# Optimization experiments

Measured on AMD Instinct MI355X. Metric: run time of the kernel, lower is better.

Reference implementation:

```python
import jax, jax.numpy as jnp
import numpy as np

NA, NT = 50000, 100000          # address / transaction node counts
FA, FT = 128, 64                # raw feature dims per node type
HID, OUT, HEADS, NCLS = 128, 64, 8, 2
E1, E2 = 500000, 250000         # cross-type / same-type edge counts
NEG_SLOPE = 0.2
LN_EPS = 1e-5


def _edge_att(xs, xd, src, dst, a_s, a_d, n_dst):
    # xs: [Ns,H,D] projected src feats, xd: [Nd,H,D] projected dst feats
    alpha_s = (xs * a_s).sum(-1)                     # [Ns,H]
    alpha_d = (xd * a_d).sum(-1)                     # [Nd,H]
    alpha = alpha_s[src] + alpha_d[dst]              # [E,H]
    alpha = jnp.where(alpha > 0, alpha, NEG_SLOPE * alpha)  # leaky_relu(0.2)
    # segment softmax over incoming edges of each dst node
    m = jax.lax.stop_gradient(jax.ops.segment_max(alpha, dst, num_segments=n_dst))
    m = jnp.where(jnp.isfinite(m), m, 0.0)
    ex = jnp.exp(alpha - m[dst])
    denom = jax.ops.segment_sum(ex, dst, num_segments=n_dst)
    w = ex / jnp.maximum(denom[dst], 1e-16)          # [E,H]
    msg = xs[src] * w[:, :, None]                    # [E,H,D]
    out = jax.ops.segment_sum(msg, dst, num_segments=n_dst)
    return jax.nn.relu(out.reshape(n_dst, -1))       # [Nd, H*D] (HANConv relu per edge type)


def _group(outs, q, kW, kb):
    # semantic-level attention over metapaths; outs: [K,N,F]
    score = (jnp.tanh(outs @ kW + kb).mean(axis=1) * q).sum(-1)  # [K]
    attn = jax.nn.softmax(score)
    return jnp.einsum('k,knf->nf', attn, outs)


def _layer_norm(x, g, b):
    mu = x.mean(-1, keepdims=True)
    var = ((x - mu) ** 2).mean(-1, keepdims=True)
    return (x - mu) / jnp.sqrt(var + LN_EPS) * g + b


def _han_conv(xa, xt, edges, Wa, ba, Wt, bt, atts, q, kW, kb):
    C = Wa.shape[1]
    D = C // HEADS
    za = (xa @ Wa + ba).reshape(-1, HEADS, D)
    zt = (xt @ Wt + bt).reshape(-1, HEADS, D)
    (eat_s, eat_d), (eta_s, eta_d), (eaa_s, eaa_d), (ett_s, ett_d) = edges
    (as_at, ad_at), (as_ta, ad_ta), (as_aa, ad_aa), (as_tt, ad_tt) = atts
    o_at = _edge_att(za, zt, eat_s, eat_d, as_at, ad_at, zt.shape[0])  # -> transaction
    o_ta = _edge_att(zt, za, eta_s, eta_d, as_ta, ad_ta, za.shape[0])  # -> address
    o_aa = _edge_att(za, za, eaa_s, eaa_d, as_aa, ad_aa, za.shape[0])  # -> address
    o_tt = _edge_att(zt, zt, ett_s, ett_d, as_tt, ad_tt, zt.shape[0])  # -> transaction
    new_a = _group(jnp.stack([o_ta, o_aa]), q, kW, kb)
    new_t = _group(jnp.stack([o_at, o_tt]), q, kW, kb)
    return new_a, new_t


def _forward(x_address, x_transaction,
             W_a1, b_a1, W_t1, b_t1,
             as_at1, ad_at1, as_ta1, ad_ta1, as_aa1, ad_aa1, as_tt1, ad_tt1,
             k1_W, k1_b, q1,
             W_a2, b_a2, W_t2, b_t2,
             as_at2, ad_at2, as_ta2, ad_ta2, as_aa2, ad_aa2, as_tt2, ad_tt2,
             k2_W, k2_b, q2,
             ln1_g, ln1_b, ln2_g, ln2_b, lin_W, lin_b, edges):
    atts1 = ((as_at1, ad_at1), (as_ta1, ad_ta1), (as_aa1, ad_aa1), (as_tt1, ad_tt1))
    atts2 = ((as_at2, ad_at2), (as_ta2, ad_ta2), (as_aa2, ad_aa2), (as_tt2, ad_tt2))
    xa, xt = _han_conv(x_address, x_transaction, edges, W_a1, b_a1, W_t1, b_t1, atts1, q1, k1_W, k1_b)
    xa = jax.nn.relu(_layer_norm(xa, ln1_g, ln1_b))
    xt = jax.nn.relu(_layer_norm(xt, ln1_g, ln1_b))
    # dropout is identity in eval mode
    xa, xt = _han_conv(xa, xt, edges, W_a2, b_a2, W_t2, b_t2, atts2, q2, k2_W, k2_b)
    xa = jax.nn.relu(_layer_norm(xa, ln2_g, ln2_b))
    return xa @ lin_W + lin_b                          # [NA, NCLS]


def setup_inputs() -> dict:
    key = jax.random.key(0)
    ks = jax.random.split(key, 40)
    D1, D2 = HID // HEADS, OUT // HEADS
    def n(i, shape, s=0.1):
        return jax.random.normal(ks[i], shape, jnp.float32) * s
    inp = {
        'x_address': jax.random.normal(ks[0], (NA, FA), jnp.float32),
        'x_transaction': jax.random.normal(ks[1], (NT, FT), jnp.float32),
        'eat_src': jax.random.randint(ks[2], (E1,), 0, NA),
        'eat_dst': jax.random.randint(ks[3], (E1,), 0, NT),
        'eta_src': jax.random.randint(ks[4], (E1,), 0, NT),
        'eta_dst': jax.random.randint(ks[5], (E1,), 0, NA),
        'eaa_src': jax.random.randint(ks[6], (E2,), 0, NA),
        'eaa_dst': jax.random.randint(ks[7], (E2,), 0, NA),
        'ett_src': jax.random.randint(ks[8], (E2,), 0, NT),
        'ett_dst': jax.random.randint(ks[9], (E2,), 0, NT),
        'W_a1': n(10, (FA, HID)), 'b_a1': jnp.zeros((HID,), jnp.float32),
        'W_t1': n(11, (FT, HID)), 'b_t1': jnp.zeros((HID,), jnp.float32),
        'as_at1': n(12, (HEADS, D1)), 'ad_at1': n(13, (HEADS, D1)),
        'as_ta1': n(14, (HEADS, D1)), 'ad_ta1': n(15, (HEADS, D1)),
        'as_aa1': n(16, (HEADS, D1)), 'ad_aa1': n(17, (HEADS, D1)),
        'as_tt1': n(18, (HEADS, D1)), 'ad_tt1': n(19, (HEADS, D1)),
        'k1_W': n(20, (HID, HID)), 'k1_b': jnp.zeros((HID,), jnp.float32), 'q1': n(21, (HID,)),
        'W_a2': n(22, (HID, OUT)), 'b_a2': jnp.zeros((OUT,), jnp.float32),
        'W_t2': n(23, (HID, OUT)), 'b_t2': jnp.zeros((OUT,), jnp.float32),
        'as_at2': n(24, (HEADS, D2)), 'ad_at2': n(25, (HEADS, D2)),
        'as_ta2': n(26, (HEADS, D2)), 'ad_ta2': n(27, (HEADS, D2)),
        'as_aa2': n(28, (HEADS, D2)), 'ad_aa2': n(29, (HEADS, D2)),
        'as_tt2': n(30, (HEADS, D2)), 'ad_tt2': n(31, (HEADS, D2)),
        'k2_W': n(32, (OUT, OUT)), 'k2_b': jnp.zeros((OUT,), jnp.float32), 'q2': n(33, (OUT,)),
        'ln1_g': jnp.ones((HID,), jnp.float32), 'ln1_b': jnp.zeros((HID,), jnp.float32),
        'ln2_g': jnp.ones((OUT,), jnp.float32), 'ln2_b': jnp.zeros((OUT,), jnp.float32),
        'lin_W': n(34, (OUT, NCLS)), 'lin_b': jnp.zeros((NCLS,), jnp.float32),
    }
    return inp


def reference(x_address, x_transaction,
              eat_src, eat_dst, eta_src, eta_dst, eaa_src, eaa_dst, ett_src, ett_dst,
              W_a1, b_a1, W_t1, b_t1,
              as_at1, ad_at1, as_ta1, ad_ta1, as_aa1, ad_aa1, as_tt1, ad_tt1,
              k1_W, k1_b, q1,
              W_a2, b_a2, W_t2, b_t2,
              as_at2, ad_at2, as_ta2, ad_ta2, as_aa2, ad_aa2, as_tt2, ad_tt2,
              k2_W, k2_b, q2,
              ln1_g, ln1_b, ln2_g, ln2_b, lin_W, lin_b):
    edges = ((eat_src, eat_dst), (eta_src, eta_dst), (eaa_src, eaa_dst), (ett_src, ett_dst))
    return _forward(x_address, x_transaction,
                    W_a1, b_a1, W_t1, b_t1,
                    as_at1, ad_at1, as_ta1, ad_ta1, as_aa1, ad_aa1, as_tt1, ad_tt1,
                    k1_W, k1_b, q1,
                    W_a2, b_a2, W_t2, b_t2,
                    as_at2, ad_at2, as_ta2, ad_ta2, as_aa2, ad_aa2, as_tt2, ad_tt2,
                    k2_W, k2_b, q2,
                    ln1_g, ln1_b, ln2_g, ln2_b, lin_W, lin_b, edges)
```

## Files before the change

### kernel.cpp

```cpp
#include <hip/hip_runtime.h>
#include <cstdint>
#include <cstddef>
#include <type_traits>

#define NA 50000
#define NT 100000
#define FA 128
#define FT 64
#define HID 128
#define OUTF 64
#define HEADS 8
#define E1 500000
#define E2 250000
#define NTOT (2*NT + 2*NA)
#define ETOT (2*E1 + 2*E2)
#define NSH 8

typedef __attribute__((ext_vector_type(8))) short short8;
typedef __attribute__((ext_vector_type(4))) float f32x4;

static __device__ __forceinline__ ushort f2b(float f) {
  unsigned int u = __float_as_uint(f);
  return (ushort)((u + 0x7fffu + ((u >> 16) & 1u)) >> 16);
}
static __device__ __forceinline__ float b2f(ushort b) {
  return __uint_as_float(((unsigned int)b) << 16);
}
static __device__ __forceinline__ float u2f_lo(unsigned int u) {
  return __uint_as_float(u << 16);
}
static __device__ __forceinline__ float u2f_hi(unsigned int u) {
  return __uint_as_float(u & 0xffff0000u);
}

template<int KK>
static __device__ __forceinline__ int lidx(int row, int off) {
  return row * KK + (off ^ ((row & 7) << 3));
}

template<int KK, int M>
static __device__ __forceinline__ void stageB(const float* __restrict__ W,
                                              ushort* __restrict__ Bls)
{
  constexpr int TPC = 256 / M;
  constexpr int CH  = KK / TPC;
  constexpr int BL  = (CH < 16) ? CH : 16;
  int t = threadIdx.x;
  int col = t % M;
  int k0 = (t / M) * CH;
  const float* Wp = W + col;
#pragma unroll
  for (int b = 0; b < CH; b += BL) {
    float v[BL];
#pragma unroll
    for (int i = 0; i < BL; i++) v[i] = Wp[(size_t)(k0 + b + i) * M];
#pragma unroll
    for (int q = 0; q < BL / 8; q++) {
      union { ushort u[8]; uint4 x; } p;
#pragma unroll
      for (int i = 0; i < 8; i++) p.u[i] = f2b(v[q * 8 + i]);
      *reinterpret_cast<uint4*>(&Bls[lidx<KK>(col, k0 + b + q * 8)]) = p.x;
    }
  }
}

template<int KK, typename AT>
struct ARegs {
  float4 f[std::is_same<AT, float>::value ? KK / 16 : 1];
  uint4  u[std::is_same<AT, float>::value ? 1 : KK / 32];
};

template<int KK, typename AT>
static __device__ __forceinline__ void loadA(const AT* __restrict__ A, int N,
                                             int row0, ARegs<KK, AT>& R)
{
  int t = threadIdx.x;
  int arow = t >> 2, ac0 = (t & 3) * (KK / 4);
  int row = row0 + arow;
  bool ok = row < N;
  const AT* Ap = A + (size_t)row * KK + ac0;
  if constexpr (std::is_same<AT, float>::value) {
#pragma unroll
    for (int j = 0; j < KK / 16; j++)
      R.f[j] = ok ? *reinterpret_cast<const float4*>(Ap + j * 4)
                  : make_float4(0.f, 0.f, 0.f, 0.f);
  } else {
#pragma unroll
    for (int j = 0; j < KK / 32; j++)
      R.u[j] = ok ? *reinterpret_cast<const uint4*>(Ap + j * 8)
                  : make_uint4(0, 0, 0, 0);
  }
}

template<int KK, typename AT>
static __device__ __forceinline__ void writeA(const ARegs<KK, AT>& R,
                                              ushort* __restrict__ Als)
{
  int t = threadIdx.x;
  int arow = t >> 2, ac0 = (t & 3) * (KK / 4);
#pragma unroll
  for (int j = 0; j < KK / 32; j++) {
    uint4 w;
    if constexpr (std::is_same<AT, float>::value) {
      union { ushort u[8]; uint4 x; } p;
      float4 a0 = R.f[2 * j], a1 = R.f[2 * j + 1];
      p.u[0] = f2b(a0.x); p.u[1] = f2b(a0.y); p.u[2] = f2b(a0.z); p.u[3] = f2b(a0.w);
      p.u[4] = f2b(a1.x); p.u[5] = f2b(a1.y); p.u[6] = f2b(a1.z); p.u[7] = f2b(a1.w);
      w = p.x;
    } else {
      w = R.u[j];
    }
    *reinterpret_cast<uint4*>(&Als[lidx<KK>(arow, ac0 + j * 8)]) = w;
  }
}

template<int KK, int NCT>
static __device__ __forceinline__ void mfma_tile(const ushort* __restrict__ Als,
    const ushort* __restrict__ Bls, f32x4* acc)
{
  int lane = threadIdx.x & 63, w = threadIdx.x >> 6;
  int l15 = lane & 15, l4 = lane >> 4;
#pragma unroll
  for (int ks = 0; ks < KK / 32; ks++) {
    short8 af = *reinterpret_cast<const short8*>(
        &Als[lidx<KK>(16 * w + l15, ks * 32 + l4 * 8)]);
#pragma unroll
    for (int n = 0; n < NCT; n++) {
      short8 bf = *reinterpret_cast<const short8*>(
          &Bls[lidx<KK>(16 * n + l15, ks * 32 + l4 * 8)]);
      acc[n] = __builtin_amdgcn_mfma_f32_16x16x32_bf16(af, bf, acc[n], 0, 0, 0);
    }
  }
}

template<int NV, int DD, int KK, int M, int TPB, typename AT>
__global__ __launch_bounds__(256) void zgemm_k(
    const AT* __restrict__ A, const float* __restrict__ W,
    const float* __restrict__ bias,
    const float* __restrict__ v0, const float* __restrict__ v1,
    const float* __restrict__ v2, const float* __restrict__ v3,
    float* __restrict__ o0, float* __restrict__ o1,
    float* __restrict__ o2, float* __restrict__ o3,
    ushort* __restrict__ Cb, int N)
{
  constexpr int NCT = M / 16;
  __shared__ __align__(16) ushort Bls[M * KK];
  __shared__ __align__(16) ushort Als[64 * KK];
  int t = threadIdx.x, w = t >> 6, lane = t & 63;
  int l15 = lane & 15, l4 = lane >> 4;
  int ntiles = (N + 63) >> 6;
  int tile0 = blockIdx.x * TPB;
  int nt = min(TPB, ntiles - tile0);

  stageB<KK, M>(W, Bls);
  ARegs<KK, AT> R;
  loadA<KK, AT>(A, N, tile0 * 64, R);

  float bv[NCT], aw0[NCT], aw1[NCT], aw2[NCT], aw3[NCT];
#pragma unroll
  for (int n = 0; n < NCT; n++) {
    int col = 16 * n + l15;
    bv[n] = bias[col];
    int head = (DD == 16) ? n : (n * 2 + (l15 >> 3));
    int vi = head * DD + (l15 & (DD - 1));
    aw0[n] = v0[vi];
    aw1[n] = (NV > 1) ? v1[vi] : 0.f;
    aw2[n] = (NV > 2) ? v2[vi] : 0.f;
    aw3[n] = (NV > 3) ? v3[vi] : 0.f;
  }

  for (int i = 0; i < nt; i++) {
    int row0 = (tile0 + i) * 64;
    __syncthreads();
    writeA<KK, AT>(R, Als);
    __syncthreads();
    if (i + 1 < nt) loadA<KK, AT>(A, N, row0 + 64, R);
    f32x4 acc[NCT];
#pragma unroll
    for (int n = 0; n < NCT; n++) acc[n] = (f32x4){0.f, 0.f, 0.f, 0.f};
    mfma_tile<KK, NCT>(Als, Bls, acc);

#pragma unroll
    for (int n = 0; n < NCT; n++) {
      int col = 16 * n + l15;
      int head = (DD == 16) ? n : (n * 2 + (l15 >> 3));
#pragma unroll
      for (int r = 0; r < 4; r++) {
        int row = row0 + 16 * w + l4 * 4 + r;
        float v = acc[n][r] + bv[n];
        if (row < N) Cb[(size_t)row * M + col] = f2b(v);
        float a0 = v * aw0[n], a1 = v * aw1[n], a2 = v * aw2[n], a3 = v * aw3[n];
#pragma unroll
        for (int o = 1; o < DD; o <<= 1) {
          a0 += __shfl_xor(a0, o);
          if (NV > 1) a1 += __shfl_xor(a1, o);
          if (NV > 2) a2 += __shfl_xor(a2, o);
          if (NV > 3) a3 += __shfl_xor(a3, o);
        }
        if ((l15 & (DD - 1)) == 0 && row < N) {
          o0[(size_t)row * 8 + head] = a0;
          if (NV > 1) o1[(size_t)row * 8 + head] = a1;
          if (NV > 2) o2[(size_t)row * 8 + head] = a2;
          if (NV > 3) o3[(size_t)row * 8 + head] = a3;
        }
      }
    }
  }
}

template<int KK, int M, int TPB>
__global__ __launch_bounds__(256) void score_k(
    const ushort* __restrict__ A0, const ushort* __restrict__ A1,
    const ushort* __restrict__ A2, const ushort* __restrict__ A3,
    const float* __restrict__ W, const float* __restrict__ bias,
    const float* __restrict__ qv, float* __restrict__ scp,
    int4 cumB, int4 Ns)
{
  constexpr int NCT = M / 16;
  __shared__ __align__(16) ushort Bls[M * KK];
  __shared__ __align__(16) ushort Als[64 * KK];
  __shared__ float red[4];
  int b = blockIdx.x;
  int tsk, bbase, N; const ushort* A;
  if      (b < cumB.x) { tsk = 0; bbase = 0;      N = Ns.x; A = A0; }
  else if (b < cumB.y) { tsk = 1; bbase = cumB.x; N = Ns.y; A = A1; }
  else if (b < cumB.z) { tsk = 2; bbase = cumB.y; N = Ns.z; A = A2; }
  else                 { tsk = 3; bbase = cumB.z; N = Ns.w; A = A3; }
  int t = threadIdx.x, w = t >> 6, lane = t & 63;
  int l15 = lane & 15, l4 = lane >> 4;
  int ntiles = (N + 63) >> 6;
  int tile0 = (b - bbase) * TPB;
  int nt = min(TPB, ntiles - tile0);

  stageB<KK, M>(W, Bls);
  ARegs<KK, ushort> R;
  loadA<KK, ushort>(A, N, tile0 * 64, R);

  float bb[NCT], qb[NCT];
#pragma unroll
  for (int n = 0; n < NCT; n++) {
    int col = 16 * n + l15;
    bb[n] = bias[col]; qb[n] = qv[col];
  }

  float ls = 0.f;
  for (int i = 0; i < nt; i++) {
    int row0 = (tile0 + i) * 64;
    __syncthreads();
    writeA<KK, ushort>(R, Als);
    __syncthreads();
    if (i + 1 < nt) loadA<KK, ushort>(A, N, row0 + 64, R);
    f32x4 acc[NCT];
#pragma unroll
    for (int n = 0; n < NCT; n++) acc[n] = (f32x4){0.f, 0.f, 0.f, 0.f};
    mfma_tile<KK, NCT>(Als, Bls, acc);
#pragma unroll
    for (int n = 0; n < NCT; n++) {
#pragma unroll
      for (int r = 0; r < 4; r++) {
        int row = row0 + 16 * w + l4 * 4 + r;
        if (row < N) ls += tanhf(acc[n][r] + bb[n]) * qb[n];
      }
    }
  }
#pragma unroll
  for (int o = 32; o > 0; o >>= 1) ls += __shfl_xor(ls, o);
  if (lane == 0) red[w] = ls;
  __syncthreads();
  if (t == 0) atomicAdd(&scp[tsk], red[0] + red[1] + red[2] + red[3]);
}

__global__ void hist4_sh(const int* __restrict__ d0, const int* __restrict__ d1,
    const int* __restrict__ d2, const int* __restrict__ d3,
    int* __restrict__ cnt8, float* __restrict__ scp)
{
  if (blockIdx.x == 0 && threadIdx.x < 8) scp[threadIdx.x] = 0.f;
  int e = blockIdx.x * 256 + threadIdx.x;
  int sh = blockIdx.x & (NSH - 1);
  int d;
  if      (e < E1)          d = d0[e];
  else if (e < 2*E1)        d = d1[e - E1] + NT;
  else if (e < 2*E1 + E2)   d = d2[e - 2*E1] + NT + NA;
  else if (e < ETOT)        d = d3[e - 2*E1 - E2] + NT + 2*NA;
  else return;
  atomicAdd(&cnt8[sh * NTOT + d], 1);
}

__global__ void scatter_sh(const int* __restrict__ s0, const int* __restrict__ d0,
    const int* __restrict__ s1, const int* __restrict__ d1,
    const int* __restrict__ s2, const int* __restrict__ d2,
    const int* __restrict__ s3, const int* __restrict__ d3,
    int* __restrict__ cur8, int* __restrict__ ssh)
{
  int e = blockIdx.x * 256 + threadIdx.x;
  int sh = blockIdx.x & (NSH - 1);
  int d, s;
  if      (e < E1)          { d = d0[e];                           s = s0[e]; }
  else if (e < 2*E1)        { d = d1[e - E1] + NT;                 s = s1[e - E1]; }
  else if (e < 2*E1 + E2)   { d = d2[e - 2*E1] + NT + NA;          s = s2[e - 2*E1]; }
  else if (e < ETOT)        { d = d3[e - 2*E1 - E2] + NT + 2*NA;   s = s3[e - 2*E1 - E2]; }
  else return;
  int p = atomicAdd(&cur8[sh * NTOT + d], 1);
  ssh[p] = s;
}

__global__ void compact_k(const int* __restrict__ rp8, const int* __restrict__ rp,
    const int* __restrict__ ssh, int* __restrict__ ssrc)
{
  int g = blockIdx.x * 256 + threadIdx.x;
  if (g >= NTOT) return;
  int w = rp[g];
#pragma unroll
  for (int s = 0; s < NSH; s++) {
    int b0 = rp8[s * NTOT + g], b1 = rp8[s * NTOT + g + 1];
    for (int e = b0; e < b1; e++) ssrc[w++] = ssh[e];
  }
}

__global__ __launch_bounds__(256) void scan_blk(const int* __restrict__ in,
    int* __restrict__ rp1, int* __restrict__ bsum, int n)
{
  __shared__ int sh[256];
  int base = blockIdx.x * 2048;
  int t = threadIdx.x;
  int v[8]; int s = 0;
#pragma unroll
  for (int k = 0; k < 8; k++) {
    int i = base + t * 8 + k;
    v[k] = (i < n) ? in[i] : 0; s += v[k];
  }
  sh[t] = s; __syncthreads();
  for (int o = 1; o < 256; o <<= 1) {
    int x = (t >= o) ? sh[t - o] : 0;
    __syncthreads(); sh[t] += x; __syncthreads();
  }
  int run = (t == 0) ? 0 : sh[t - 1];
  if (t == 255 && bsum) bsum[blockIdx.x] = sh[255];
#pragma unroll
  for (int k = 0; k < 8; k++) {
    int i = base + t * 8 + k;
    run += v[k];
    if (i < n) rp1[i] = run;
  }
}

__global__ __launch_bounds__(256) void scan_blk_sum8(const int* __restrict__ cnt8,
    int* __restrict__ rp1, int* __restrict__ bsum, int n)
{
  __shared__ int sh[256];
  int base = blockIdx.x * 2048;
  int t = threadIdx.x;
  int v[8]; int s = 0;
#pragma unroll
  for (int k = 0; k < 8; k++) {
    int i = base + t * 8 + k;
    int x = 0;
    if (i < n) {
#pragma unroll
      for (int sh2 = 0; sh2 < NSH; sh2++) x += cnt8[sh2 * NTOT + i];
    }
    v[k] = x; s += x;
  }
  sh[t] = s; __syncthreads();
  for (int o = 1; o < 256; o <<= 1) {
    int x = (t >= o) ? sh[t - o] : 0;
    __syncthreads(); sh[t] += x; __syncthreads();
  }
  int run = (t == 0) ? 0 : sh[t - 1];
  if (t == 255 && bsum) bsum[blockIdx.x] = sh[255];
#pragma unroll
  for (int k = 0; k < 8; k++) {
    int i = base + t * 8 + k;
    run += v[k];
    if (i < n) rp1[i] = run;
  }
}

__global__ __launch_bounds__(256) void scan_two(int* __restrict__ b0, int n0,
                                                int* __restrict__ b1, int n1)
{
  __shared__ int sh[256];
  int* arr = blockIdx.x ? b1 : b0;
  int n = blockIdx.x ? n1 : n0;
  int t = threadIdx.x;
  int v[8]; int s = 0;
#pragma unroll
  for (int k = 0; k < 8; k++) {
    int i = t * 8 + k;
    v[k] = (i < n) ? arr[i] : 0; s += v[k];
  }
  sh[t] = s; __syncthreads();
  for (int o = 1; o < 256; o <<= 1) {
    int x = (t >= o) ? sh[t - o] : 0;
    __syncthreads(); sh[t] += x; __syncthreads();
  }
  int run = (t == 0) ? 0 : sh[t - 1];
#pragma unroll
  for (int k = 0; k < 8; k++) {
    int i = t * 8 + k;
    run += v[k];
    if (i < n) arr[i] = run;
  }
}

__global__ void scan_add2(int* __restrict__ rp, int* __restrict__ cur,
    const int* __restrict__ bsA, int n)
{
  int i = blockIdx.x * blockDim.x + threadIdx.x;
  if (i == 0) { rp[0] = 0; cur[0] = 0; }
  if (i < n) {
    int blk = i >> 11;
    int base = blk ? bsA[blk - 1] : 0;
    int v = rp[i + 1] + base;
    rp[i + 1] = v;
    if (i + 1 < n) cur[i + 1] = v;
  }
}

__global__ void scan_add(int* __restrict__ rp, const int* __restrict__ bsA, int n)
{
  int i = blockIdx.x * blockDim.x + threadIdx.x;
  if (i == 0) rp[0] = 0;
  if (i < n) {
    int blk = i >> 11;
    int base = blk ? bsA[blk - 1] : 0;
    rp[i + 1] += base;
  }
}

struct AggTask {
  int g0, Nd;
  const float* als; const float* ald;
  const ushort* z;  ushort* out;
};

template<int F>
__global__ __launch_bounds__(256) void agg_multi(const int* __restrict__ rp,
    const int* __restrict__ ssrc, AggTask C0A, AggTask C0B,
    AggTask C1A, AggTask C1B, int split0, int split1, int btot)
{
  constexpr int LPN = (F == 128) ? 16 : 8;
  constexpr int NPW = 64 / LPN;
  int b = blockIdx.x;
  int cls = (b >> 2) & 1;
  int lb = (b >> 3) * 4 + (b & 3);
  if (lb >= btot) return;
  AggTask T;
  if (cls == 0) { if (lb < split0) T = C0A; else { T = C0B; lb -= split0; } }
  else          { if (lb < split1) T = C1A; else { T = C1B; lb -= split1; } }
  int wv = threadIdx.x >> 6, lane = threadIdx.x & 63;
  int grp = lane / LPN, lg = lane % LPN;
  int n = (lb * 4 + wv) * NPW + grp;
  if (n >= T.Nd) return;
  int g = T.g0 + n;
  int start = rp[g], end = rp[g + 1];
  int hh = (F == 128) ? (lg >> 1) : lg;
  float ad_h = T.ald[(size_t)n * 8 + hh];

  float den = 0.f;
  float acc[8] = {};
  int e = start;
  for (; e + 1 < end; e += 2) {
    int sn0 = ssrc[e], sn1 = ssrc[e + 1];
    uint4 z0 = *reinterpret_cast<const uint4*>(T.z + (size_t)sn0 * F + lg * 8);
    uint4 z1 = *reinterpret_cast<const uint4*>(T.z + (size_t)sn1 * F + lg * 8);
    float a0 = T.als[(size_t)sn0 * 8 + hh] + ad_h;
    float a1 = T.als[(size_t)sn1 * 8 + hh] + ad_h;
    a0 = a0 > 0.f ? a0 : 0.2f * a0;
    a1 = a1 > 0.f ? a1 : 0.2f * a1;
    float p0 = __expf(fminf(a0, 30.f));
    float p1 = __expf(fminf(a1, 30.f));
    den += p0 + p1;
    acc[0] = fmaf(p0, u2f_lo(z0.x), fmaf(p1, u2f_lo(z1.x), acc[0]));
    acc[1] = fmaf(p0, u2f_hi(z0.x), fmaf(p1, u2f_hi(z1.x), acc[1]));
    acc[2] = fmaf(p0, u2f_lo(z0.y), fmaf(p1, u2f_lo(z1.y), acc[2]));
    acc[3] = fmaf(p0, u2f_hi(z0.y), fmaf(p1, u2f_hi(z1.y), acc[3]));
    acc[4] = fmaf(p0, u2f_lo(z0.z), fmaf(p1, u2f_lo(z1.z), acc[4]));
    acc[5] = fmaf(p0, u2f_hi(z0.z), fmaf(p1, u2f_hi(z1.z), acc[5]));
    acc[6] = fmaf(p0, u2f_lo(z0.w), fmaf(p1, u2f_lo(z1.w), acc[6]));
    acc[7] = fmaf(p0, u2f_hi(z0.w), fmaf(p1, u2f_hi(z1.w), acc[7]));
  }
  if (e < end) {
    int sn = ssrc[e];
    uint4 zv = *reinterpret_cast<const uint4*>(T.z + (size_t)sn * F + lg * 8);
    float a = T.als[(size_t)sn * 8 + hh] + ad_h;
    a = a > 0.f ? a : 0.2f * a;
    float p = __expf(fminf(a, 30.f));
    den += p;
    acc[0] = fmaf(p, u2f_lo(zv.x), acc[0]);
    acc[1] = fmaf(p, u2f_hi(zv.x), acc[1]);
    acc[2] = fmaf(p, u2f_lo(zv.y), acc[2]);
    acc[3] = fmaf(p, u2f_hi(zv.y), acc[3]);
    acc[4] = fmaf(p, u2f_lo(zv.z), acc[4]);
    acc[5] = fmaf(p, u2f_hi(zv.z), acc[5]);
    acc[6] = fmaf(p, u2f_lo(zv.w), acc[6]);
    acc[7] = fmaf(p, u2f_hi(zv.w), acc[7]);
  }
  float inv = 1.f / fmaxf(den, 1e-16f);
  unsigned int pk[4];
#pragma unroll
  for (int k2 = 0; k2 < 4; k2++)
    pk[k2] = (unsigned int)f2b(fmaxf(acc[2*k2] * inv, 0.f))
           | ((unsigned int)f2b(fmaxf(acc[2*k2+1] * inv, 0.f)) << 16);
  *reinterpret_cast<uint4*>(T.out + (size_t)n * F + lg * 8)
      = make_uint4(pk[0], pk[1], pk[2], pk[3]);
}

__global__ __launch_bounds__(256) void combine2_k(
    const ushort* __restrict__ o00, const ushort* __restrict__ o01,
    const float* __restrict__ sc0, float invn0, ushort* __restrict__ out0, int N0,
    const ushort* __restrict__ o10, const ushort* __restrict__ o11,
    const float* __restrict__ sc1, float invn1, ushort* __restrict__ out1, int N1,
    const float* __restrict__ g, const float* __restrict__ bb)
{
  int c1 = (N0 + 3) / 4;
  int b = blockIdx.x;
  const ushort *o0, *o1; const float* sc; float invn; ushort* outp; int N, lb;
  if (b < c1) { o0=o00; o1=o01; sc=sc0; invn=invn0; outp=out0; N=N0; lb=b; }
  else        { o0=o10; o1=o11; sc=sc1; invn=invn1; outp=out1; N=N1; lb=b-c1; }
  int wv = threadIdx.x >> 6, lane = threadIdx.x & 63;
  int n = lb * 4 + wv;
  if (n >= N) return;
  float s0 = sc[0] * invn, s1 = sc[1] * invn;
  float mx = fmaxf(s0, s1);
  float e0 = __expf(s0 - mx), e1 = __expf(s1 - mx);
  float w0 = e0 / (e0 + e1), w1 = e1 / (e0 + e1);
  float x[2];
#pragma unroll
  for (int jj = 0; jj < 2; jj++) {
    int idx = lane + 64 * jj;
    x[jj] = w0 * b2f(o0[(size_t)n * 128 + idx]) + w1 * b2f(o1[(size_t)n * 128 + idx]);
  }
  float sum = x[0] + x[1];
#pragma unroll
  for (int o = 32; o > 0; o >>= 1) sum += __shfl_xor(sum, o);
  float mu = sum / 128.f;
  float vs = 0.f;
#pragma unroll
  for (int jj = 0; jj < 2; jj++) { float dd = x[jj] - mu; vs = fmaf(dd, dd, vs); }
#pragma unroll
  for (int o = 32; o > 0; o >>= 1) vs += __shfl_xor(vs, o);
  float rstd = rsqrtf(vs / 128.f + 1e-5f);
#pragma unroll
  for (int jj = 0; jj < 2; jj++) {
    int idx = lane + 64 * jj;
    float y = (x[jj] - mu) * rstd * g[idx] + bb[idx];
    outp[(size_t)n * 128 + idx] = f2b(fmaxf(y, 0.f));
  }
}

__global__ __launch_bounds__(256) void combine_final_k(
    const ushort* __restrict__ o0, const ushort* __restrict__ o1,
    const float* __restrict__ sc, float invn,
    const float* __restrict__ g, const float* __restrict__ bb,
    const float* __restrict__ lw, const float* __restrict__ lb,
    float* __restrict__ outp, int N)
{
  int wv = threadIdx.x >> 6, lane = threadIdx.x & 63;
  int n = blockIdx.x * 4 + wv;
  if (n >= N) return;
  float s0 = sc[0] * invn, s1 = sc[1] * invn;
  float mx = fmaxf(s0, s1);
  float e0 = __expf(s0 - mx), e1 = __expf(s1 - mx);
  float w0 = e0 / (e0 + e1), w1 = e1 / (e0 + e1);
  float x = w0 * b2f(o0[(size_t)n * 64 + lane]) + w1 * b2f(o1[(size_t)n * 64 + lane]);
  float sum = x;
#pragma unroll
  for (int o = 32; o > 0; o >>= 1) sum += __shfl_xor(sum, o);
  float mu = sum / 64.f;
  float dd = x - mu;
  float vs = dd * dd;
#pragma unroll
  for (int o = 32; o > 0; o >>= 1) vs += __shfl_xor(vs, o);
  float rstd = rsqrtf(vs / 64.f + 1e-5f);
  float y = fmaxf((x - mu) * rstd * g[lane] + bb[lane], 0.f);
  float p0 = y * lw[lane * 2 + 0];
  float p1 = y * lw[lane * 2 + 1];
#pragma unroll
  for (int o = 32; o > 0; o >>= 1) { p0 += __shfl_xor(p0, o); p1 += __shfl_xor(p1, o); }
  if (lane == 0) {
    outp[(size_t)n * 2 + 0] = p0 + lb[0];
    outp[(size_t)n * 2 + 1] = p1 + lb[1];
  }
}

extern "C" void kernel_launch(void* const* d_in, const int* in_sizes, int n_in,
                              void* d_out, int out_size, void* d_ws, size_t ws_size,
                              hipStream_t stream)
{
  (void)in_sizes; (void)n_in; (void)out_size;
  const float* x_a = (const float*)d_in[0];
  const float* x_t = (const float*)d_in[1];
  const int* eat_s = (const int*)d_in[2];
  const int* eat_d = (const int*)d_in[3];
  const int* eta_s = (const int*)d_in[4];
  const int* eta_d = (const int*)d_in[5];
  const int* eaa_s = (const int*)d_in[6];
  const int* eaa_d = (const int*)d_in[7];
  const int* ett_s = (const int*)d_in[8];
  const int* ett_d = (const int*)d_in[9];
  const float* W_a1 = (const float*)d_in[10]; const float* b_a1 = (const float*)d_in[11];
  const float* W_t1 = (const float*)d_in[12]; const float* b_t1 = (const float*)d_in[13];
  const float* as_at1 = (const float*)d_in[14]; const float* ad_at1 = (const float*)d_in[15];
  const float* as_ta1 = (const float*)d_in[16]; const float* ad_ta1 = (const float*)d_in[17];
  const float* as_aa1 = (const float*)d_in[18]; const float* ad_aa1 = (const float*)d_in[19];
  const float* as_tt1 = (const float*)d_in[20]; const float* ad_tt1 = (const float*)d_in[21];
  const float* k1_W = (const float*)d_in[22]; const float* k1_b = (const float*)d_in[23];
  const float* q1   = (const float*)d_in[24];
  const float* W_a2 = (const float*)d_in[25]; const float* b_a2 = (const float*)d_in[26];
  const float* W_t2 = (const float*)d_in[27]; const float* b_t2 = (const float*)d_in[28];
  const float* as_ta2 = (const float*)d_in[31]; const float* ad_ta2 = (const float*)d_in[32];
  const float* as_aa2 = (const float*)d_in[33]; const float* ad_aa2 = (const float*)d_in[34];
  const float* k2_W = (const float*)d_in[37]; const float* k2_b = (const float*)d_in[38];
  const float* q2   = (const float*)d_in[39];
  const float* ln1_g = (const float*)d_in[40]; const float* ln1_b = (const float*)d_in[41];
  const float* ln2_g = (const float*)d_in[42]; const float* ln2_b = (const float*)d_in[43];
  const float* lin_W = (const float*)d_in[44]; const float* lin_b = (const float*)d_in[45];

  char* ws = (char*)d_ws;
  size_t off = 0;
  auto alloc = [&](size_t bytes) {
    size_t o = off; off += (bytes + 255) & ~(size_t)255; return o;
  };
  size_t ZA1 = alloc((size_t)NA * HID * 2);
  size_t ZT1 = alloc((size_t)NT * HID * 2);
  size_t OTA = alloc((size_t)NA * HID * 2);
  size_t OAA = alloc((size_t)NA * HID * 2);
  size_t OAT = alloc((size_t)NT * HID * 2);
  size_t OTT = alloc((size_t)NT * HID * 2);
  size_t A_AS_AT = alloc((size_t)NA * 8 * 4);
  size_t A_AD_TA = alloc((size_t)NA * 8 * 4);
  size_t A_AS_AA = alloc((size_t)NA * 8 * 4);
  size_t A_AD_AA = alloc((size_t)NA * 8 * 4);
  size_t A_T_D_AT = alloc((size_t)NT * 8 * 4);
  size_t A_T_S_TA = alloc((size_t)NT * 8 * 4);
  size_t A_T_S_TT = alloc((size_t)NT * 8 * 4);
  size_t A_T_D_TT = alloc((size_t)NT * 8 * 4);
  size_t RP8  = alloc(((size_t)NSH * NTOT + 1) * 4);
  size_t CUR8 = alloc((size_t)NSH * NTOT * 4);
  size_t SSH  = alloc((size_t)ETOT * 4);
  size_t RP   = alloc((size_t)(NTOT + 1) * 4);
  size_t SS   = alloc((size_t)ETOT * 4);
  size_t BSM  = alloc(2048 * 4);
  size_t BSM2 = alloc(256 * 4);
  size_t SC   = alloc(256);
  if (off > ws_size) return;

  ushort* za1 = (ushort*)(ws + ZA1);
  ushort* zt1 = (ushort*)(ws + ZT1);
  ushort* ota = (ushort*)(ws + OTA);
  ushort* oaa = (ushort*)(ws + OAA);
  ushort* oat = (ushort*)(ws + OAT);
  ushort* ott = (ushort*)(ws + OTT);
  float* aASAT = (float*)(ws + A_AS_AT);
  float* aADTA = (float*)(ws + A_AD_TA);
  float* aASAA = (float*)(ws + A_AS_AA);
  float* aADAA = (float*)(ws + A_AD_AA);
  float* aTDAT = (float*)(ws + A_T_D_AT);
  float* aTSTA = (float*)(ws + A_T_S_TA);
  float* aTSTT = (float*)(ws + A_T_S_TT);
  float* aTDTT = (float*)(ws + A_T_D_TT);
  int* rp8  = (int*)(ws + RP8);
  int* cur8 = (int*)(ws + CUR8);
  int* ssh  = (int*)(ws + SSH);
  int* rp   = (int*)(ws + RP);
  int* ssrc = (int*)(ws + SS);
  int* bsum = (int*)(ws + BSM);
  int* bsum2= (int*)(ws + BSM2);
  float* scp = (float*)(ws + SC);
  ushort* za2 = za1;
  ushort* zt2 = zt1;
  ushort* ota2 = oaa;
  ushort* oaa2 = (ushort*)(ws + OAA + (size_t)NA * OUTF * 2);

  const int TA = (NA + 63) / 64, TT = (NT + 63) / 64;
  const int EBL = (ETOT + 255) / 256;
  const int SCN8 = NSH * NTOT;
  const int SBL8 = (SCN8 + 2047) / 2048;
  const int SBL1 = (NTOT + 2047) / 2048;

  hipMemsetAsync(cur8, 0, (size_t)SCN8 * 4, stream);
  hist4_sh<<<EBL, 256, 0, stream>>>(eat_d, eta_d, eaa_d, ett_d, cur8, scp);
  scan_blk<<<SBL8, 256, 0, stream>>>(cur8, rp8 + 1, bsum, SCN8);
  scan_blk_sum8<<<SBL1, 256, 0, stream>>>(cur8, rp + 1, bsum2, NTOT);
  scan_two<<<2, 256, 0, stream>>>(bsum, SBL8, bsum2, SBL1);
  scan_add2<<<(SCN8 + 255) / 256, 256, 0, stream>>>(rp8, cur8, bsum, SCN8);
  scan_add<<<(NTOT + 255) / 256, 256, 0, stream>>>(rp, bsum2, NTOT);
  scatter_sh<<<EBL, 256, 0, stream>>>(eat_s, eat_d, eta_s, eta_d,
                                      eaa_s, eaa_d, ett_s, ett_d, cur8, ssh);
  compact_k<<<(NTOT + 255) / 256, 256, 0, stream>>>(rp8, rp, ssh, ssrc);

  zgemm_k<4,16,FA,HID,2,float><<<(TA+1)/2,256,0,stream>>>(x_a, W_a1, b_a1,
      as_at1, ad_ta1, as_aa1, ad_aa1, aASAT, aADTA, aASAA, aADAA, za1, NA);
  zgemm_k<4,16,FT,HID,4,float><<<(TT+3)/4,256,0,stream>>>(x_t, W_t1, b_t1,
      ad_at1, as_ta1, as_tt1, ad_tt1, aTDAT, aTSTA, aTSTT, aTDTT, zt1, NT);
  {
    const int BT = (NT + 15) / 16, BA = (NA + 15) / 16;
    const int btot = BT + BA;
    const int grid = ((btot + 3) / 4) * 8;
    AggTask Tat{0,        NT, aASAT, aTDAT, za1, oat};
    AggTask Taa{NT+NA,    NA, aASAA, aADAA, za1, oaa};
    AggTask Tta{NT,       NA, aTSTA, aADTA, zt1, ota};
    AggTask Ttt{NT+2*NA,  NT, aTSTT, aTDTT, zt1, ott};
    agg_multi<128><<<grid, 256, 0, stream>>>(rp, ssrc,
        Tat, Taa, Tta, Ttt, BT, BA, btot);
  }
  {
    const int bA = (TA + 3) / 4, bT = (TT + 3) / 4;
    score_k<HID,HID,4><<<2*bA + 2*bT, 256, 0, stream>>>(ota, oaa, oat, ott,
        k1_W, k1_b, q1, scp,
        make_int4(bA, 2*bA, 2*bA + bT, 2*bA + 2*bT),
        make_int4(NA, NA, NT, NT));
  }
  combine2_k<<<(NA/4) + (NT/4), 256, 0, stream>>>(
      ota, oaa, scp + 0, 1.f/NA, ota, NA,
      oat, ott, scp + 2, 1.f/NT, oat, NT, ln1_g, ln1_b);

  zgemm_k<3,8,HID,OUTF,2,ushort><<<(TA+1)/2,256,0,stream>>>(ota, W_a2, b_a2,
      ad_ta2, as_aa2, ad_aa2, nullptr, aADTA, aASAA, aADAA, nullptr, za2, NA);
  zgemm_k<1,8,HID,OUTF,4,ushort><<<(TT+3)/4,256,0,stream>>>(oat, W_t2, b_t2,
      as_ta2, nullptr, nullptr, nullptr, aTSTA, nullptr, nullptr, nullptr, zt2, NT);
  {
    const int BA2 = (NA + 31) / 32;
    const int grid = ((BA2 + 3) / 4) * 8;
    AggTask Taa2{NT+NA, NA, aASAA, aADAA, za2, oaa2};
    AggTask Tta2{NT,    NA, aTSTA, aADTA, zt2, ota2};
    agg_multi<64><<<grid, 256, 0, stream>>>(rp, ssrc,
        Taa2, Taa2, Tta2, Tta2, BA2, BA2, BA2);
  }
  {
    const int bA = (TA + 3) / 4;
    score_k<OUTF,OUTF,4><<<2*bA, 256, 0, stream>>>(ota2, oaa2, ota2, ota2,
        k2_W, k2_b, q2, scp + 4,
        make_int4(bA, 2*bA, 2*bA, 2*bA),
        make_int4(NA, NA, NA, NA));
  }
  combine_final_k<<<NA/4, 256, 0, stream>>>(ota2, oaa2, scp + 4, 1.f/NA,
      ln2_g, ln2_b, lin_W, lin_b, (float*)d_out, NA);
}
```

Baseline: 519.0 us.

## Sort destination nodes by degree to balance aggregation work across wavefronts

Adds a counting sort of destination nodes by in-degree (capped at 64 buckets) per segment, producing a permutation that the aggregation kernels use to map lanes to nodes. Nodes with similar degree then share a wavefront, which reduces divergence and idle lanes in the edge loop. It also merges the two scan-add kernels into one launch. The cost is three extra small kernels with atomics plus an indirect node lookup, and the permutation breaks the locality of output and dst-attention accesses.

```diff
diff --git a/kernel.cpp b/kernel.cpp
--- a/kernel.cpp
+++ b/kernel.cpp
@@ -15,6 +15,7 @@
 #define NTOT (2*NT + 2*NA)
 #define ETOT (2*E1 + 2*E2)
 #define NSH 8
+#define NDB 64
 
 typedef __attribute__((ext_vector_type(8))) short short8;
 typedef __attribute__((ext_vector_type(4))) float f32x4;
@@ -403,29 +404,67 @@
   }
 }
 
-__global__ void scan_add2(int* __restrict__ rp, int* __restrict__ cur,
-    const int* __restrict__ bsA, int n)
+__global__ void scan_addM(int* __restrict__ rp8, int* __restrict__ cur8,
+    const int* __restrict__ bsA, int n8,
+    int* __restrict__ rp, const int* __restrict__ bsB, int n1)
 {
   int i = blockIdx.x * blockDim.x + threadIdx.x;
-  if (i == 0) { rp[0] = 0; cur[0] = 0; }
-  if (i < n) {
+  if (i == 0) { rp8[0] = 0; cur8[0] = 0; rp[0] = 0; }
+  if (i < n8) {
     int blk = i >> 11;
     int base = blk ? bsA[blk - 1] : 0;
-    int v = rp[i + 1] + base;
-    rp[i + 1] = v;
-    if (i + 1 < n) cur[i + 1] = v;
-  }
-}
-
-__global__ void scan_add(int* __restrict__ rp, const int* __restrict__ bsA, int n)
-{
-  int i = blockIdx.x * blockDim.x + threadIdx.x;
-  if (i == 0) rp[0] = 0;
-  if (i < n) {
+    int v = rp8[i + 1] + base;
+    rp8[i + 1] = v;
+    if (i + 1 < n8) cur8[i + 1] = v;
+  }
+  if (i < n1) {
     int blk = i >> 11;
-    int base = blk ? bsA[blk - 1] : 0;
+    int base = blk ? bsB[blk - 1] : 0;
     rp[i + 1] += base;
   }
+}
+
+static __device__ __forceinline__ void seg_of(int g, int& segbase) {
+  if      (g < NT)          segbase = 0;
+  else if (g < NT + NA)     segbase = NT;
+  else if (g < NT + 2*NA)   segbase = NT + NA;
+  else                      segbase = NT + 2*NA;
+}
+static __device__ __forceinline__ int segid_of(int g) {
+  if      (g < NT)          return 0;
+  else if (g < NT + NA)     return 1;
+  else if (g < NT + 2*NA)   return 2;
+  else                      return 3;
+}
+
+__global__ void deg_hist(const int* __restrict__ rp, int* __restrict__ dh)
+{
+  int g = blockIdx.x * 256 + threadIdx.x;
+  if (g >= NTOT) return;
+  int deg = min(rp[g + 1] - rp[g], NDB - 1);
+  atomicAdd(&dh[segid_of(g) * NDB + deg], 1);
+}
+
+__global__ void deg_scan(int* __restrict__ dh)
+{
+  int s = threadIdx.x;
+  if (s < 4) {
+    int run = 0;
+    for (int d = 0; d < NDB; d++) {
+      int c = dh[s * NDB + d]; dh[s * NDB + d] = run; run += c;
+    }
+  }
+}
+
+__global__ void deg_scat(const int* __restrict__ rp, int* __restrict__ dcur,
+                         int* __restrict__ perm)
+{
+  int g = blockIdx.x * 256 + threadIdx.x;
+  if (g >= NTOT) return;
+  int segbase; seg_of(g, segbase);
+  int deg = min(rp[g + 1] - rp[g], NDB - 1);
+  int pos = atomicAdd(&dcur[segid_of(g) * NDB + deg], 1);
+  perm[segbase + pos] = g - segbase;
 }
 
 struct AggTask {
@@ -436,8 +475,9 @@
 
 template<int F>
 __global__ __launch_bounds__(256) void agg_multi(const int* __restrict__ rp,
-    const int* __restrict__ ssrc, AggTask C0A, AggTask C0B,
-    AggTask C1A, AggTask C1B, int split0, int split1, int btot)
+    const int* __restrict__ ssrc, const int* __restrict__ perm,
+    AggTask C0A, AggTask C0B, AggTask C1A, AggTask C1B,
+    int split0, int split1, int btot)
 {
   constexpr int LPN = (F == 128) ? 16 : 8;
   constexpr int NPW = 64 / LPN;
@@ -450,8 +490,9 @@
   else          { if (lb < split1) T = C1A; else { T = C1B; lb -= split1; } }
   int wv = threadIdx.x >> 6, lane = threadIdx.x & 63;
   int grp = lane / LPN, lg = lane % LPN;
-  int n = (lb * 4 + wv) * NPW + grp;
-  if (n >= T.Nd) return;
+  int idx = (lb * 4 + wv) * NPW + grp;
+  if (idx >= T.Nd) return;
+  int n = perm[T.g0 + idx];
   int g = T.g0 + n;
   int start = rp[g], end = rp[g + 1];
   int hh = (F == 128) ? (lg >> 1) : lg;
@@ -643,6 +684,8 @@
   size_t SS   = alloc((size_t)ETOT * 4);
   size_t BSM  = alloc(2048 * 4);
   size_t BSM2 = alloc(256 * 4);
+  size_t DH   = alloc(4 * NDB * 4);
+  size_t PERM = alloc((size_t)NTOT * 4);
   size_t SC   = alloc(256);
   if (off > ws_size) return;
 
@@ -667,6 +710,8 @@
   int* ssrc = (int*)(ws + SS);
   int* bsum = (int*)(ws + BSM);
   int* bsum2= (int*)(ws + BSM2);
+  int* dh   = (int*)(ws + DH);
+  int* perm = (int*)(ws + PERM);
   float* scp = (float*)(ws + SC);
   ushort* za2 = za1;
   ushort* zt2 = zt1;
@@ -678,17 +723,22 @@
   const int SCN8 = NSH * NTOT;
   const int SBL8 = (SCN8 + 2047) / 2048;
   const int SBL1 = (NTOT + 2047) / 2048;
+  const int NBL = (NTOT + 255) / 256;
 
   hipMemsetAsync(cur8, 0, (size_t)SCN8 * 4, stream);
+  hipMemsetAsync(dh, 0, 4 * NDB * 4, stream);
   hist4_sh<<<EBL, 256, 0, stream>>>(eat_d, eta_d, eaa_d, ett_d, cur8, scp);
   scan_blk<<<SBL8, 256, 0, stream>>>(cur8, rp8 + 1, bsum, SCN8);
   scan_blk_sum8<<<SBL1, 256, 0, stream>>>(cur8, rp + 1, bsum2, NTOT);
   scan_two<<<2, 256, 0, stream>>>(bsum, SBL8, bsum2, SBL1);
-  scan_add2<<<(SCN8 + 255) / 256, 256, 0, stream>>>(rp8, cur8, bsum, SCN8);
-  scan_add<<<(NTOT + 255) / 256, 256, 0, stream>>>(rp, bsum2, NTOT);
+  scan_addM<<<(SCN8 + 255) / 256, 256, 0, stream>>>(rp8, cur8, bsum, SCN8,
+                                                    rp, bsum2, NTOT);
   scatter_sh<<<EBL, 256, 0, stream>>>(eat_s, eat_d, eta_s, eta_d,
                                       eaa_s, eaa_d, ett_s, ett_d, cur8, ssh);
-  compact_k<<<(NTOT + 255) / 256, 256, 0, stream>>>(rp8, rp, ssh, ssrc);
+  compact_k<<<NBL, 256, 0, stream>>>(rp8, rp, ssh, ssrc);
+  deg_hist<<<NBL, 256, 0, stream>>>(rp, dh);
+  deg_scan<<<1, 64, 0, stream>>>(dh);
+  deg_scat<<<NBL, 256, 0, stream>>>(rp, dh, perm);
 
   zgemm_k<4,16,FA,HID,2,float><<<(TA+1)/2,256,0,stream>>>(x_a, W_a1, b_a1,
       as_at1, ad_ta1, as_aa1, ad_aa1, aASAT, aADTA, aASAA, aADAA, za1, NA);
@@ -702,7 +752,7 @@
     AggTask Taa{NT+NA,    NA, aASAA, aADAA, za1, oaa};
     AggTask Tta{NT,       NA, aTSTA, aADTA, zt1, ota};
     AggTask Ttt{NT+2*NA,  NT, aTSTT, aTDTT, zt1, ott};
-    agg_multi<128><<<grid, 256, 0, stream>>>(rp, ssrc,
+    agg_multi<128><<<grid, 256, 0, stream>>>(rp, ssrc, perm,
         Tat, Taa, Tta, Ttt, BT, BA, btot);
   }
   {
@@ -725,7 +775,7 @@
     const int grid = ((BA2 + 3) / 4) * 8;
     AggTask Taa2{NT+NA, NA, aASAA, aADAA, za2, oaa2};
     AggTask Tta2{NT,    NA, aTSTA, aADTA, zt2, ota2};
-    agg_multi<64><<<grid, 256, 0, stream>>>(rp, ssrc,
+    agg_multi<64><<<grid, 256, 0, stream>>>(rp, ssrc, perm,
         Taa2, Taa2, Tta2, Tta2, BA2, BA2, BA2);
   }
   {
```

After: 1.725 ms. +232.4%, slower.
